# Optimization experiments

Measured on AMD Instinct MI355X. Metric: run time of the kernel, lower is better.

The kernel has to match this reference:

```python
import jax, jax.numpy as jnp
import numpy as np
from jax import lax

WIN = 11
SIGMA = 1.5
C1 = 0.01 ** 2
C2 = 0.03 ** 2


def _gauss_window(c):
    x = np.arange(WIN) - WIN // 2
    g = np.exp(-(x ** 2) / (2.0 * SIGMA ** 2))
    g = g / g.sum()
    w2d = np.outer(g, g).astype(np.float32)  # [11,11]
    return jnp.asarray(np.broadcast_to(w2d, (c, 1, WIN, WIN)).copy())


def _dwconv(x, kernel, groups):
    # x: [B,C,H,W], kernel: [C,1,kh,kw] depthwise, stride 1, SAME padding
    return lax.conv_general_dilated(
        x, kernel, window_strides=(1, 1), padding='SAME',
        dimension_numbers=('NCHW', 'OIHW', 'NCHW'),
        feature_group_count=groups)


_SOBEL_X = jnp.asarray(np.array([[-1, 0, 1], [-2, 0, 2], [-1, 0, 1]], np.float32))
_SOBEL_Y = jnp.asarray(np.array([[1, 2, 1], [0, 0, 0], [-1, -2, -1]], np.float32))


def _sobel_xy(x):
    # x: [B,3,H,W] -> depthwise 3x3 sobel on each channel (same as per-channel conv2d)
    c = x.shape[1]
    kx = jnp.broadcast_to(_SOBEL_X, (c, 1, 3, 3))
    ky = jnp.broadcast_to(_SOBEL_Y, (c, 1, 3, 3))
    return _dwconv(x, kx, c), _dwconv(x, ky, c)


def _rgb2ycrcb(im):
    R, G, B = im[:, 0:1], im[:, 1:2], im[:, 2:3]
    Y = 0.299 * R + 0.587 * G + 0.114 * B
    Cr = (R - Y) * 0.713 + 0.5
    Cb = (B - Y) * 0.564 + 0.5
    return Y, Cr, Cb


def _ssim(img1, img2, channel):
    w = _gauss_window(channel)
    mu1 = _dwconv(img1, w, channel)
    mu2 = _dwconv(img2, w, channel)
    mu1_sq = mu1 * mu1
    mu2_sq = mu2 * mu2
    mu12 = mu1 * mu2
    s1 = _dwconv(img1 * img1, w, channel) - mu1_sq
    s2 = _dwconv(img2 * img2, w, channel) - mu2_sq
    s12 = _dwconv(img1 * img2, w, channel) - mu12
    ssim_map = ((2 * mu12 + C1) * (2 * s12 + C2)) / ((mu1_sq + mu2_sq + C1) * (s1 + s2 + C2))
    return ssim_map.mean()


def _l1(a, b):
    return jnp.mean(jnp.abs(a - b))


def setup_inputs() -> dict:
    key = jax.random.key(0)
    k1, k2, k3 = jax.random.split(key, 3)
    shp = (16, 3, 512, 512)
    return {
        'input_vis': jax.random.uniform(k1, shp, jnp.float32),
        'input_ir': jax.random.uniform(k2, shp, jnp.float32),
        'fuse': jax.random.uniform(k3, shp, jnp.float32),
    }


def reference(input_vis, input_ir, fuse):
    # color components
    _, Cr_F, Cb_F = _rgb2ycrcb(fuse)
    _, Cr_V, Cb_V = _rgb2ycrcb(input_vis)
    Y_ir = input_ir[:, 0:1]

    # sobel gradients (depthwise over 3 channels == per-channel conv + cat)
    Fgx, Fgy = _sobel_xy(fuse)
    Vgx, Vgy = _sobel_xy(input_vis)
    Igx, Igy = _sobel_xy(input_ir)
    joint_gx = jnp.maximum(Vgx, Igx)
    joint_gy = jnp.maximum(Vgy, Igy)
    joint_int = jnp.maximum(input_vis, input_ir)

    con_loss = _l1(fuse, joint_int)
    gradient_loss = 0.5 * _l1(Fgx, joint_gx) + 0.5 * _l1(Fgy, joint_gy)
    color_loss = _l1(Cb_F, Cb_V) + _l1(Cr_F, Cr_V)

    # SSIM: rgb-vs-fused (3ch) and ir-Y vs gray(fused) (1ch)
    ssim_rgb = _ssim(input_vis, fuse, 3)
    gray_fused = (0.2989 * fuse[:, 0:1] + 0.587 * fuse[:, 1:2] + 0.114 * fuse[:, 2:3])
    ssim_ir = _ssim(Y_ir, gray_fused, 1)
    ssim_loss = 1.0 - (ssim_rgb + ssim_ir) / 2.0

    return 0.5 * con_loss + 0.2 * gradient_loss + 1.0 * color_loss + 0.1 * ssim_loss
```

## Files before the change

### kernel.cpp

```cpp
#include <hip/hip_runtime.h>

#define IMG_H 512
#define IMG_W 512
#define CH_STRIDE (IMG_H*IMG_W)
#define IMG_STRIDE (3*CH_STRIDE)

using f4 = __attribute__((ext_vector_type(4))) float;
using h4 = __attribute__((ext_vector_type(4))) _Float16;

#define NSLOT 64
#define SLOT_F 32

__global__ __launch_bounds__(256) void k_zero(float* __restrict__ acc) {
  int i = threadIdx.x;
  *(f4*)&acc[i*8]     = f4{0,0,0,0};
  *(f4*)&acc[i*8 + 4] = f4{0,0,0,0};
}

__device__ __forceinline__ float block_sum(float v, float* red) {
  #pragma unroll
  for (int o = 32; o > 0; o >>= 1) v += __shfl_down(v, o, 64);
  __syncthreads();
  if ((threadIdx.x & 63) == 0) red[threadIdx.x >> 6] = v;
  __syncthreads();
  return red[0] + red[1] + red[2] + red[3];
}

#define R1W 68
#define R1N (18*R1W)

#define SXW 80
#define SXH 42
#define HBW 68
#define HBN (SXH*HBW)

#define SMEM_BYTES 36288

__global__ __launch_bounds__(256, 4) void k_main(
    const float* __restrict__ vis, const float* __restrict__ ir,
    const float* __restrict__ fuse, float* __restrict__ acc)
{
  __shared__ __align__(16) char smem[SMEM_BYTES];
  __shared__ float red[4];
  const int tid = threadIdx.x;
  const int bid = blockIdx.x;
  float* aslot = acc + (bid & (NSLOT-1))*SLOT_F;

  if (bid < 8192) {
    const int z = bid >> 7;
    const int n = z >> 2, pair = z & 3;
    const int x0 = (bid & 7)*64;
    const int y0 = ((bid >> 3) & 15)*32;
    _Float16* sx = (_Float16*)smem;
    _Float16* sy = (_Float16*)(smem + 6720);
    _Float16* hA = (_Float16*)(smem + 13440);
    _Float16* hB = (_Float16*)(smem + 19152);
    _Float16* hP = (_Float16*)(smem + 24864);
    _Float16* hQ = (_Float16*)(smem + 30576);

    float g[11];
    {
      const float gu[6] = {0.00386592014f, 0.02856550078f, 0.13533528324f,
                           0.41111229050f, 0.80073740292f, 1.0f};
      float gs = 0.f;
      #pragma unroll
      for (int i = 0; i < 11; ++i) { g[i] = gu[i < 6 ? i : 10 - i]; gs += g[i]; }
      #pragma unroll
      for (int i = 0; i < 11; ++i) g[i] /= gs;
    }

    if (pair < 3) {
      const float* xb = vis  + (n*3 + pair)*CH_STRIDE;
      const float* yb = fuse + (n*3 + pair)*CH_STRIDE;
      for (int i = tid; i < SXH*20; i += 256) {
        int row = i / 20, k = i - row*20;
        int gy = y0 - 5 + row, gx = x0 - 8 + 4*k;
        f4 xv = {0,0,0,0}, yv = {0,0,0,0};
        if ((unsigned)gx < IMG_W && (unsigned)gy < IMG_H) {
          int off = gy*IMG_W + gx;
          xv = *(const f4*)&xb[off];
          yv = *(const f4*)&yb[off];
        }
        int ib = row*SXW + 4*k;
        *(h4*)&sx[ib] = h4{(_Float16)xv.x,(_Float16)xv.y,(_Float16)xv.z,(_Float16)xv.w};
        *(h4*)&sy[ib] = h4{(_Float16)yv.x,(_Float16)yv.y,(_Float16)yv.z,(_Float16)yv.w};
      }
    } else {
      const float* xb = ir   + n*IMG_STRIDE;
      const float* fb = fuse + n*IMG_STRIDE;
      for (int i = tid; i < SXH*20; i += 256) {
        int row = i / 20, k = i - row*20;
        int gy = y0 - 5 + row, gx = x0 - 8 + 4*k;
        f4 xv = {0,0,0,0}, yv = {0,0,0,0};
        if ((unsigned)gx < IMG_W && (unsigned)gy < IMG_H) {
          int off = gy*IMG_W + gx;
          xv = *(const f4*)&xb[off];
          f4 rr = *(const f4*)&fb[off];
          f4 gg = *(const f4*)&fb[off + CH_STRIDE];
          f4 bb = *(const f4*)&fb[off + 2*CH_STRIDE];
          #pragma unroll
          for (int j = 0; j < 4; ++j)
            yv[j] = 0.2989f*rr[j] + 0.587f*gg[j] + 0.114f*bb[j];
        }
        int ib = row*SXW + 4*k;
        *(h4*)&sx[ib] = h4{(_Float16)xv.x,(_Float16)xv.y,(_Float16)xv.z,(_Float16)xv.w};
        *(h4*)&sy[ib] = h4{(_Float16)yv.x,(_Float16)yv.y,(_Float16)yv.z,(_Float16)yv.w};
      }
    }
    __syncthreads();

    for (int gi = tid; gi < SXH*16; gi += 256) {
      int row = gi >> 4, gox = (gi & 15)*4;
      int base = row*SXW + gox;
      float wa[20], wb[20];
      #pragma unroll
      for (int u = 0; u < 5; ++u) {
        h4 av = *(const h4*)&sx[base + 4*u];
        h4 bv = *(const h4*)&sy[base + 4*u];
        #pragma unroll
        for (int j = 0; j < 4; ++j) { wa[4*u+j] = (float)av[j]; wb[4*u+j] = (float)bv[j]; }
      }
      float wp[14], wq[14];
      #pragma unroll
      for (int u = 0; u < 14; ++u) {
        float a = wa[u+3], b = wb[u+3];
        wp[u] = fmaf(a, a, b*b);
        wq[u] = a*b;
      }
      float hA4[4]={0,0,0,0}, hB4[4]={0,0,0,0}, hP4[4]={0,0,0,0}, hQ4[4]={0,0,0,0};
      #pragma unroll
      for (int k = 0; k < 11; ++k) {
        float gk = g[k];
        #pragma unroll
        for (int j = 0; j < 4; ++j) {
          hA4[j] = fmaf(gk, wa[k+j+3], hA4[j]);
          hB4[j] = fmaf(gk, wb[k+j+3], hB4[j]);
          hP4[j] = fmaf(gk, wp[k+j], hP4[j]);
          hQ4[j] = fmaf(gk, wq[k+j], hQ4[j]);
        }
      }
      int ob = row*HBW + gox;
      *(h4*)&hA[ob] = h4{(_Float16)hA4[0],(_Float16)hA4[1],(_Float16)hA4[2],(_Float16)hA4[3]};
      *(h4*)&hB[ob] = h4{(_Float16)hB4[0],(_Float16)hB4[1],(_Float16)hB4[2],(_Float16)hB4[3]};
      *(h4*)&hP[ob] = h4{(_Float16)hP4[0],(_Float16)hP4[1],(_Float16)hP4[2],(_Float16)hP4[3]};
      *(h4*)&hQ[ob] = h4{(_Float16)hQ4[0],(_Float16)hQ4[1],(_Float16)hQ4[2],(_Float16)hQ4[3]};
    }
    __syncthreads();

    const int vox = (tid & 15)*4;
    const int yb2 = (tid >> 4)*2;
    float aA0[4]={0,0,0,0}, aA1[4]={0,0,0,0};
    float aB0[4]={0,0,0,0}, aB1[4]={0,0,0,0};
    float aP0[4]={0,0,0,0}, aP1[4]={0,0,0,0};
    float aQ0[4]={0,0,0,0}, aQ1[4]={0,0,0,0};
    #pragma unroll
    for (int r = 0; r < 12; ++r) {
      int rb = (yb2 + r)*HBW + vox;
      h4 fA = *(const h4*)&hA[rb];
      h4 fB = *(const h4*)&hB[rb];
      h4 fP = *(const h4*)&hP[rb];
      h4 fQ = *(const h4*)&hQ[rb];
      if (r < 11) {
        float gk = g[r];
        #pragma unroll
        for (int j = 0; j < 4; ++j) {
          aA0[j] = fmaf(gk, (float)fA[j], aA0[j]);
          aB0[j] = fmaf(gk, (float)fB[j], aB0[j]);
          aP0[j] = fmaf(gk, (float)fP[j], aP0[j]);
          aQ0[j] = fmaf(gk, (float)fQ[j], aQ0[j]);
        }
      }
      if (r >= 1) {
        float gk = g[r-1];
        #pragma unroll
        for (int j = 0; j < 4; ++j) {
          aA1[j] = fmaf(gk, (float)fA[j], aA1[j]);
          aB1[j] = fmaf(gk, (float)fB[j], aB1[j]);
          aP1[j] = fmaf(gk, (float)fP[j], aP1[j]);
          aQ1[j] = fmaf(gk, (float)fQ[j], aQ1[j]);
        }
      }
    }

    float ss = 0.f;
    #pragma unroll
    for (int j = 0; j < 4; ++j) {
      {
        float mu1 = aA0[j], mu2 = aB0[j];
        float mu12 = mu1*mu2, mss = mu1*mu1 + mu2*mu2;
        float s12 = aQ0[j] - mu12, sps = aP0[j] - mss;
        ss += ((2.f*mu12 + 1e-4f)*(2.f*s12 + 9e-4f)) / ((mss + 1e-4f)*(sps + 9e-4f));
      }
      {
        float mu1 = aA1[j], mu2 = aB1[j];
        float mu12 = mu1*mu2, mss = mu1*mu1 + mu2*mu2;
        float s12 = aQ1[j] - mu12, sps = aP1[j] - mss;
        ss += ((2.f*mu12 + 1e-4f)*(2.f*s12 + 9e-4f)) / ((mss + 1e-4f)*(sps + 9e-4f));
      }
    }
    float tot = block_sum(ss, red);
    if (tid == 0) atomicAdd(&aslot[(pair == 3) ? 6 : 5], tot);

  } else {
    const int r = bid - 8192;
    const int x0 = (r & 7)*64;
    const int y0 = ((r >> 3) & 31)*16;
    const int n  = r >> 8;
    float* s = (float*)smem;
    const int ox = (tid & 15)*4;
    const int oy = tid >> 4;

    float con=0.f, gxs=0.f, gys=0.f, cbs=0.f, crs=0.f;
    float pv[3][4], pf[3][4];

    for (int c = 0; c < 3; ++c) {
      const float* pv0 = vis  + (n*3 + c)*CH_STRIDE;
      const float* pi0 = ir   + (n*3 + c)*CH_STRIDE;
      const float* pf0 = fuse + (n*3 + c)*CH_STRIDE;
      for (int i = tid; i < 864; i += 256) {
        int f = i / 288;
        int rr = i - f*288;
        int row = rr >> 4, k = rr & 15;
        int gy = y0 - 1 + row, gx = x0 + 4*k;
        f4 v = {0,0,0,0};
        const float* bp = (f == 0) ? pv0 : ((f == 1) ? pi0 : pf0);
        if ((unsigned)gy < IMG_H) v = *(const f4*)&bp[gy*IMG_W + gx];
        float* dst = s + f*R1N + row*R1W + 1 + 4*k;
        dst[0]=v.x; dst[1]=v.y; dst[2]=v.z; dst[3]=v.w;
      }
      if (tid < 108) {
        int f = tid / 36;
        int rr = tid - f*36;
        int row = rr >> 1, side = rr & 1;
        int gy = y0 - 1 + row;
        int gx = side ? (x0 + 64) : (x0 - 1);
        float v = 0.f;
        const float* bp = (f == 0) ? pv0 : ((f == 1) ? pi0 : pf0);
        if ((unsigned)gx < IMG_W && (unsigned)gy < IMG_H) v = bp[gy*IMG_W + gx];
        s[f*R1N + row*R1W + (side ? 65 : 0)] = v;
      }
      __syncthreads();

      float cen[3][4], gxv[3][4], gyv[3][4];
      #pragma unroll
      for (int t = 0; t < 3; ++t) {
        const float* sf = s + t*R1N;
        float r0[8], r1[8], r2[8];
        {
          f4 a = *(const f4*)&sf[(oy+0)*R1W + ox], b = *(const f4*)&sf[(oy+0)*R1W + ox + 4];
          r0[0]=a.x; r0[1]=a.y; r0[2]=a.z; r0[3]=a.w; r0[4]=b.x; r0[5]=b.y; r0[6]=b.z; r0[7]=b.w;
        }
        {
          f4 a = *(const f4*)&sf[(oy+1)*R1W + ox], b = *(const f4*)&sf[(oy+1)*R1W + ox + 4];
          r1[0]=a.x; r1[1]=a.y; r1[2]=a.z; r1[3]=a.w; r1[4]=b.x; r1[5]=b.y; r1[6]=b.z; r1[7]=b.w;
        }
        {
          f4 a = *(const f4*)&sf[(oy+2)*R1W + ox], b = *(const f4*)&sf[(oy+2)*R1W + ox + 4];
          r2[0]=a.x; r2[1]=a.y; r2[2]=a.z; r2[3]=a.w; r2[4]=b.x; r2[5]=b.y; r2[6]=b.z; r2[7]=b.w;
        }
        #pragma unroll
        for (int j = 0; j < 4; ++j) {
          gxv[t][j] = (r0[j+2]-r0[j]) + 2.f*(r1[j+2]-r1[j]) + (r2[j+2]-r2[j]);
          gyv[t][j] = (r0[j] + 2.f*r0[j+1] + r0[j+2]) - (r2[j] + 2.f*r2[j+1] + r2[j+2]);
          cen[t][j] = r1[j+1];
        }
      }
      #pragma unroll
      for (int j = 0; j < 4; ++j) {
        con += fabsf(cen[2][j] - fmaxf(cen[0][j], cen[1][j]));
        gxs += fabsf(gxv[2][j] - fmaxf(gxv[0][j], gxv[1][j]));
        gys += fabsf(gyv[2][j] - fmaxf(gyv[0][j], gyv[1][j]));
        pv[c][j] = cen[0][j];
        pf[c][j] = cen[2][j];
      }
      __syncthreads();
    }

    #pragma unroll
    for (int j = 0; j < 4; ++j) {
      float Yf = 0.299f*pf[0][j] + 0.587f*pf[1][j] + 0.114f*pf[2][j];
      float Yv = 0.299f*pv[0][j] + 0.587f*pv[1][j] + 0.114f*pv[2][j];
      crs += fabsf(0.713f*((pf[0][j]-Yf) - (pv[0][j]-Yv)));
      cbs += fabsf(0.564f*((pf[2][j]-Yf) - (pv[2][j]-Yv)));
    }

    float r0 = block_sum(con, red);
    float r1 = block_sum(gxs, red);
    float r2 = block_sum(gys, red);
    float r3 = block_sum(cbs, red);
    float r4 = block_sum(crs, red);
    if (tid == 0) {
      atomicAdd(&aslot[0], r0);
      atomicAdd(&aslot[1], r1);
      atomicAdd(&aslot[2], r2);
      atomicAdd(&aslot[3], r3);
      atomicAdd(&aslot[4], r4);
    }
  }
}

__global__ __launch_bounds__(64) void k_final(
    const float* __restrict__ acc, float* __restrict__ out)
{
  int lane = threadIdx.x;
  float s[7];
  #pragma unroll
  for (int c = 0; c < 7; ++c) {
    float x = acc[lane*SLOT_F + c];
    #pragma unroll
    for (int o = 32; o > 0; o >>= 1) x += __shfl_down(x, o, 64);
    s[c] = x;
  }
  if (lane == 0) {
    const float N3 = 16.f*3.f*512.f*512.f;
    const float N1 = 16.f*512.f*512.f;
    float con_loss  = s[0] / N3;
    float grad_loss = 0.5f*(s[1]/N3) + 0.5f*(s[2]/N3);
    float color_loss = s[3]/N1 + s[4]/N1;
    float ssim_loss = 1.f - (s[5]/N3 + s[6]/N1)*0.5f;
    out[0] = 0.5f*con_loss + 0.2f*grad_loss + color_loss + 0.1f*ssim_loss;
  }
}

extern "C" void kernel_launch(void* const* d_in, const int* in_sizes, int n_in,
                              void* d_out, int out_size, void* d_ws, size_t ws_size,
                              hipStream_t stream) {
  (void)in_sizes; (void)n_in; (void)out_size; (void)ws_size;
  const float* vis  = (const float*)d_in[0];
  const float* ir   = (const float*)d_in[1];
  const float* fuse = (const float*)d_in[2];
  float* out = (float*)d_out;
  float* acc = (float*)d_ws;

  k_zero<<<dim3(1,1,1), dim3(256,1,1), 0, stream>>>(acc);
  k_main<<<dim3(12288,1,1), dim3(256,1,1), 0, stream>>>(vis, ir, fuse, acc);
  k_final<<<dim3(1,1,1), dim3(64,1,1), 0, stream>>>(acc, out);
}
```

Measured before the change: 255.4 us.

## Compute separable SSIM Gaussian blur with MFMA banded-matrix multiplies

```diff
diff --git a/kernel.cpp b/kernel.cpp
--- a/kernel.cpp
+++ b/kernel.cpp
@@ -7,6 +7,7 @@
 
 using f4 = __attribute__((ext_vector_type(4))) float;
 using h4 = __attribute__((ext_vector_type(4))) _Float16;
+using h8 = __attribute__((ext_vector_type(8))) _Float16;
 
 #define NSLOT 64
 #define SLOT_F 32
@@ -29,12 +30,11 @@
 #define R1W 68
 #define R1N (18*R1W)
 
-#define SXW 80
-#define SXH 42
-#define HBW 68
-#define HBN (SXH*HBW)
-
-#define SMEM_BYTES 36288
+#define FST 104
+#define FSZ (48*FST*2)
+#define HTST 72
+#define HTSZ (64*HTST*2)
+#define SMEM_BYTES (2*FSZ + 2*HTSZ)
 
 __global__ __launch_bounds__(256, 4) void k_main(
     const float* __restrict__ vis, const float* __restrict__ ir,
@@ -42,6 +42,7 @@
 {
   __shared__ __align__(16) char smem[SMEM_BYTES];
   __shared__ float red[4];
+  __shared__ float gtab[96];
   const int tid = threadIdx.x;
   const int bid = blockIdx.x;
   float* aslot = acc + (bid & (NSLOT-1))*SLOT_F;
@@ -51,12 +52,10 @@
     const int n = z >> 2, pair = z & 3;
     const int x0 = (bid & 7)*64;
     const int y0 = ((bid >> 3) & 15)*32;
-    _Float16* sx = (_Float16*)smem;
-    _Float16* sy = (_Float16*)(smem + 6720);
-    _Float16* hA = (_Float16*)(smem + 13440);
-    _Float16* hB = (_Float16*)(smem + 19152);
-    _Float16* hP = (_Float16*)(smem + 24864);
-    _Float16* hQ = (_Float16*)(smem + 30576);
+    _Float16* FX  = (_Float16*)smem;
+    _Float16* FY  = (_Float16*)(smem + FSZ);
+    _Float16* HT0 = (_Float16*)(smem + 2*FSZ);
+    _Float16* HT1 = (_Float16*)(smem + 2*FSZ + HTSZ);
 
     float g[11];
     {
@@ -72,27 +71,27 @@
     if (pair < 3) {
       const float* xb = vis  + (n*3 + pair)*CH_STRIDE;
       const float* yb = fuse + (n*3 + pair)*CH_STRIDE;
-      for (int i = tid; i < SXH*20; i += 256) {
-        int row = i / 20, k = i - row*20;
+      for (int i = tid; i < 1152; i += 256) {
+        int row = i / 24, k = i - row*24;
         int gy = y0 - 5 + row, gx = x0 - 8 + 4*k;
         f4 xv = {0,0,0,0}, yv = {0,0,0,0};
-        if ((unsigned)gx < IMG_W && (unsigned)gy < IMG_H) {
+        if ((unsigned)gy < IMG_H && (unsigned)gx < IMG_W) {
           int off = gy*IMG_W + gx;
           xv = *(const f4*)&xb[off];
           yv = *(const f4*)&yb[off];
         }
-        int ib = row*SXW + 4*k;
-        *(h4*)&sx[ib] = h4{(_Float16)xv.x,(_Float16)xv.y,(_Float16)xv.z,(_Float16)xv.w};
-        *(h4*)&sy[ib] = h4{(_Float16)yv.x,(_Float16)yv.y,(_Float16)yv.z,(_Float16)yv.w};
+        int ib = row*FST + 4*k;
+        *(h4*)&FX[ib] = h4{(_Float16)xv.x,(_Float16)xv.y,(_Float16)xv.z,(_Float16)xv.w};
+        *(h4*)&FY[ib] = h4{(_Float16)yv.x,(_Float16)yv.y,(_Float16)yv.z,(_Float16)yv.w};
       }
     } else {
       const float* xb = ir   + n*IMG_STRIDE;
       const float* fb = fuse + n*IMG_STRIDE;
-      for (int i = tid; i < SXH*20; i += 256) {
-        int row = i / 20, k = i - row*20;
+      for (int i = tid; i < 1152; i += 256) {
+        int row = i / 24, k = i - row*24;
         int gy = y0 - 5 + row, gx = x0 - 8 + 4*k;
         f4 xv = {0,0,0,0}, yv = {0,0,0,0};
-        if ((unsigned)gx < IMG_W && (unsigned)gy < IMG_H) {
+        if ((unsigned)gy < IMG_H && (unsigned)gx < IMG_W) {
           int off = gy*IMG_W + gx;
           xv = *(const f4*)&xb[off];
           f4 rr = *(const f4*)&fb[off];
@@ -102,100 +101,109 @@
           for (int j = 0; j < 4; ++j)
             yv[j] = 0.2989f*rr[j] + 0.587f*gg[j] + 0.114f*bb[j];
         }
-        int ib = row*SXW + 4*k;
-        *(h4*)&sx[ib] = h4{(_Float16)xv.x,(_Float16)xv.y,(_Float16)xv.z,(_Float16)xv.w};
-        *(h4*)&sy[ib] = h4{(_Float16)yv.x,(_Float16)yv.y,(_Float16)yv.z,(_Float16)yv.w};
-      }
+        int ib = row*FST + 4*k;
+        *(h4*)&FX[ib] = h4{(_Float16)xv.x,(_Float16)xv.y,(_Float16)xv.z,(_Float16)xv.w};
+        *(h4*)&FY[ib] = h4{(_Float16)yv.x,(_Float16)yv.y,(_Float16)yv.z,(_Float16)yv.w};
+      }
+    }
+    if (tid < 96) gtab[tid] = 0.f;
+    #pragma unroll
+    for (int k = 0; k < 11; ++k) if (tid == 40 + k) gtab[40 + k] = g[k];
+    for (int i = tid; i < 512; i += 256) {
+      _Float16* HT = (i < 256) ? HT0 : HT1;
+      int r2 = i & 255;
+      int c = r2 >> 2, rseg = 48 + (r2 & 3)*4;
+      *(h4*)&HT[c*HTST + rseg] = h4{(_Float16)0.f,(_Float16)0.f,(_Float16)0.f,(_Float16)0.f};
     }
     __syncthreads();
 
-    for (int gi = tid; gi < SXH*16; gi += 256) {
-      int row = gi >> 4, gox = (gi & 15)*4;
-      int base = row*SXW + gox;
-      float wa[20], wb[20];
-      #pragma unroll
-      for (int u = 0; u < 5; ++u) {
-        h4 av = *(const h4*)&sx[base + 4*u];
-        h4 bv = *(const h4*)&sy[base + 4*u];
+    const int w  = tid >> 6;
+    const int l  = tid & 63;
+    const int q  = l >> 4;
+    const int li = l & 15;
+
+    const int Kbase = w >> 1;
+    const int nK = 1 + (w & 1);
+    h8 gxf[2];
+    #pragma unroll
+    for (int kk = 0; kk < 2; ++kk) {
+      h8 t = {0,0,0,0,0,0,0,0};
+      if (kk < nK) {
+        int idx0 = 40 + (Kbase + kk)*32 + q*8 - w*16 - li - 3;
         #pragma unroll
-        for (int j = 0; j < 4; ++j) { wa[4*u+j] = (float)av[j]; wb[4*u+j] = (float)bv[j]; }
-      }
-      float wp[14], wq[14];
-      #pragma unroll
-      for (int u = 0; u < 14; ++u) {
-        float a = wa[u+3], b = wb[u+3];
-        wp[u] = fmaf(a, a, b*b);
-        wq[u] = a*b;
-      }
-      float hA4[4]={0,0,0,0}, hB4[4]={0,0,0,0}, hP4[4]={0,0,0,0}, hQ4[4]={0,0,0,0};
-      #pragma unroll
-      for (int k = 0; k < 11; ++k) {
-        float gk = g[k];
+        for (int j = 0; j < 8; ++j) t[j] = (_Float16)gtab[idx0 + j];
+      }
+      gxf[kk] = t;
+    }
+    h8 gyA[3];
+    {
+      const int MK[3][2] = {{0,0},{1,0},{1,1}};
+      #pragma unroll
+      for (int p = 0; p < 3; ++p) {
+        int idx0 = 40 + MK[p][1]*32 + q*8 - MK[p][0]*16 - li;
+        h8 t;
         #pragma unroll
-        for (int j = 0; j < 4; ++j) {
-          hA4[j] = fmaf(gk, wa[k+j+3], hA4[j]);
-          hB4[j] = fmaf(gk, wb[k+j+3], hB4[j]);
-          hP4[j] = fmaf(gk, wp[k+j], hP4[j]);
-          hQ4[j] = fmaf(gk, wq[k+j], hQ4[j]);
-        }
-      }
-      int ob = row*HBW + gox;
-      *(h4*)&hA[ob] = h4{(_Float16)hA4[0],(_Float16)hA4[1],(_Float16)hA4[2],(_Float16)hA4[3]};
-      *(h4*)&hB[ob] = h4{(_Float16)hB4[0],(_Float16)hB4[1],(_Float16)hB4[2],(_Float16)hB4[3]};
-      *(h4*)&hP[ob] = h4{(_Float16)hP4[0],(_Float16)hP4[1],(_Float16)hP4[2],(_Float16)hP4[3]};
-      *(h4*)&hQ[ob] = h4{(_Float16)hQ4[0],(_Float16)hQ4[1],(_Float16)hQ4[2],(_Float16)hQ4[3]};
-    }
-    __syncthreads();
-
-    const int vox = (tid & 15)*4;
-    const int yb2 = (tid >> 4)*2;
-    float aA0[4]={0,0,0,0}, aA1[4]={0,0,0,0};
-    float aB0[4]={0,0,0,0}, aB1[4]={0,0,0,0};
-    float aP0[4]={0,0,0,0}, aP1[4]={0,0,0,0};
-    float aQ0[4]={0,0,0,0}, aQ1[4]={0,0,0,0};
-    #pragma unroll
-    for (int r = 0; r < 12; ++r) {
-      int rb = (yb2 + r)*HBW + vox;
-      h4 fA = *(const h4*)&hA[rb];
-      h4 fB = *(const h4*)&hB[rb];
-      h4 fP = *(const h4*)&hP[rb];
-      h4 fQ = *(const h4*)&hQ[rb];
-      if (r < 11) {
-        float gk = g[r];
-        #pragma unroll
-        for (int j = 0; j < 4; ++j) {
-          aA0[j] = fmaf(gk, (float)fA[j], aA0[j]);
-          aB0[j] = fmaf(gk, (float)fB[j], aB0[j]);
-          aP0[j] = fmaf(gk, (float)fP[j], aP0[j]);
-          aQ0[j] = fmaf(gk, (float)fQ[j], aQ0[j]);
-        }
-      }
-      if (r >= 1) {
-        float gk = g[r-1];
-        #pragma unroll
-        for (int j = 0; j < 4; ++j) {
-          aA1[j] = fmaf(gk, (float)fA[j], aA1[j]);
-          aB1[j] = fmaf(gk, (float)fB[j], aB1[j]);
-          aP1[j] = fmaf(gk, (float)fP[j], aP1[j]);
-          aQ1[j] = fmaf(gk, (float)fQ[j], aQ1[j]);
-        }
+        for (int j = 0; j < 8; ++j) t[j] = (_Float16)gtab[idx0 + j];
+        gyA[p] = t;
+      }
+    }
+
+    f4 accF[4][2];
+    #pragma unroll
+    for (int f = 0; f < 4; ++f)
+      #pragma unroll
+      for (int m = 0; m < 2; ++m) accF[f][m] = f4{0,0,0,0};
+
+    const int cw = w*16 + li;
+
+    for (int grp = 0; grp < 2; ++grp) {
+      if (grp) __syncthreads();
+      #pragma unroll
+      for (int M = 0; M < 3; ++M) {
+        f4 c0 = {0,0,0,0}, c1 = {0,0,0,0};
+        for (int kk = 0; kk < nK; ++kk) {
+          int K = Kbase + kk;
+          int fo = (M*16 + li)*FST + K*32 + q*8;
+          h8 ax = *(const h8*)(FX + fo);
+          h8 ay = *(const h8*)(FY + fo);
+          if (grp == 0) {
+            c0 = __builtin_amdgcn_mfma_f32_16x16x32_f16(ax, gxf[kk], c0, 0, 0, 0);
+            c1 = __builtin_amdgcn_mfma_f32_16x16x32_f16(ay, gxf[kk], c1, 0, 0, 0);
+          } else {
+            h8 ap = ax*ax + ay*ay;
+            h8 aq = ax*ay;
+            c0 = __builtin_amdgcn_mfma_f32_16x16x32_f16(ap, gxf[kk], c0, 0, 0, 0);
+            c1 = __builtin_amdgcn_mfma_f32_16x16x32_f16(aq, gxf[kk], c1, 0, 0, 0);
+          }
+        }
+        int ho = cw*HTST + M*16 + q*4;
+        *(h4*)(HT0 + ho) = h4{(_Float16)c0.x,(_Float16)c0.y,(_Float16)c0.z,(_Float16)c0.w};
+        *(h4*)(HT1 + ho) = h4{(_Float16)c1.x,(_Float16)c1.y,(_Float16)c1.z,(_Float16)c1.w};
+      }
+      __syncthreads();
+      #pragma unroll
+      for (int f = 0; f < 2; ++f) {
+        const _Float16* HT = f ? HT1 : HT0;
+        int fi = grp*2 + f;
+        h8 b0 = *(const h8*)(HT + cw*HTST + q*8);
+        accF[fi][0] = __builtin_amdgcn_mfma_f32_16x16x32_f16(gyA[0], b0, accF[fi][0], 0, 0, 0);
+        accF[fi][1] = __builtin_amdgcn_mfma_f32_16x16x32_f16(gyA[1], b0, accF[fi][1], 0, 0, 0);
+        h8 b1 = *(const h8*)(HT + cw*HTST + 32 + q*8);
+        accF[fi][1] = __builtin_amdgcn_mfma_f32_16x16x32_f16(gyA[2], b1, accF[fi][1], 0, 0, 0);
       }
     }
 
     float ss = 0.f;
     #pragma unroll
-    for (int j = 0; j < 4; ++j) {
-      {
-        float mu1 = aA0[j], mu2 = aB0[j];
+    for (int M = 0; M < 2; ++M) {
+      #pragma unroll
+      for (int r = 0; r < 4; ++r) {
+        float mu1 = accF[0][M][r], mu2 = accF[1][M][r];
+        float sP  = accF[2][M][r], sQ  = accF[3][M][r];
         float mu12 = mu1*mu2, mss = mu1*mu1 + mu2*mu2;
-        float s12 = aQ0[j] - mu12, sps = aP0[j] - mss;
-        ss += ((2.f*mu12 + 1e-4f)*(2.f*s12 + 9e-4f)) / ((mss + 1e-4f)*(sps + 9e-4f));
-      }
-      {
-        float mu1 = aA1[j], mu2 = aB1[j];
-        float mu12 = mu1*mu2, mss = mu1*mu1 + mu2*mu2;
-        float s12 = aQ1[j] - mu12, sps = aP1[j] - mss;
-        ss += ((2.f*mu12 + 1e-4f)*(2.f*s12 + 9e-4f)) / ((mss + 1e-4f)*(sps + 9e-4f));
+        float s12 = sQ - mu12, sps = sP - mss;
+        ss += ((2.f*mu12 + 1e-4f)*(2.f*s12 + 9e-4f)) /
+              ((mss + 1e-4f)*(sps + 9e-4f));
       }
     }
     float tot = block_sum(ss, red);
```

New measurement: 432.6 us. +69.4%, slower.

## Interleave SSIM horizontal-blur outputs and run vertical blur in packed fp16

Applied to the files above, without the earlier changes.

```diff
diff --git a/kernel.cpp b/kernel.cpp
--- a/kernel.cpp
+++ b/kernel.cpp
@@ -7,6 +7,7 @@
 
 using f4 = __attribute__((ext_vector_type(4))) float;
 using h4 = __attribute__((ext_vector_type(4))) _Float16;
+using h8 = __attribute__((ext_vector_type(8))) _Float16;
 
 #define NSLOT 64
 #define SLOT_F 32
@@ -26,15 +27,17 @@
   return red[0] + red[1] + red[2] + red[3];
 }
 
+__device__ __forceinline__ h8 splat8(_Float16 v) { return h8{v,v,v,v,v,v,v,v}; }
+
 #define R1W 68
 #define R1N (18*R1W)
 
 #define SXW 80
 #define SXH 42
-#define HBW 68
-#define HBN (SXH*HBW)
-
-#define SMEM_BYTES 36288
+#define HB8 264
+#define SSIM_SX_B (SXH*SXW*2)
+#define SSIM_HB_B (SXH*HB8*2)
+#define SMEM_BYTES (2*SSIM_SX_B + SSIM_HB_B)
 
 __global__ __launch_bounds__(256, 4) void k_main(
     const float* __restrict__ vis, const float* __restrict__ ir,
@@ -52,13 +55,11 @@
     const int x0 = (bid & 7)*64;
     const int y0 = ((bid >> 3) & 15)*32;
     _Float16* sx = (_Float16*)smem;
-    _Float16* sy = (_Float16*)(smem + 6720);
-    _Float16* hA = (_Float16*)(smem + 13440);
-    _Float16* hB = (_Float16*)(smem + 19152);
-    _Float16* hP = (_Float16*)(smem + 24864);
-    _Float16* hQ = (_Float16*)(smem + 30576);
+    _Float16* sy = (_Float16*)(smem + SSIM_SX_B);
+    _Float16* hb = (_Float16*)(smem + 2*SSIM_SX_B);
 
     float g[11];
+    _Float16 gh[11];
     {
       const float gu[6] = {0.00386592014f, 0.02856550078f, 0.13533528324f,
                            0.41111229050f, 0.80073740292f, 1.0f};
@@ -66,7 +67,7 @@
       #pragma unroll
       for (int i = 0; i < 11; ++i) { g[i] = gu[i < 6 ? i : 10 - i]; gs += g[i]; }
       #pragma unroll
-      for (int i = 0; i < 11; ++i) g[i] /= gs;
+      for (int i = 0; i < 11; ++i) { g[i] /= gs; gh[i] = (_Float16)g[i]; }
     }
 
     if (pair < 3) {
@@ -76,7 +77,7 @@
         int row = i / 20, k = i - row*20;
         int gy = y0 - 5 + row, gx = x0 - 8 + 4*k;
         f4 xv = {0,0,0,0}, yv = {0,0,0,0};
-        if ((unsigned)gx < IMG_W && (unsigned)gy < IMG_H) {
+        if ((unsigned)gy < IMG_H && (unsigned)gx < IMG_W) {
           int off = gy*IMG_W + gx;
           xv = *(const f4*)&xb[off];
           yv = *(const f4*)&yb[off];
@@ -92,7 +93,7 @@
         int row = i / 20, k = i - row*20;
         int gy = y0 - 5 + row, gx = x0 - 8 + 4*k;
         f4 xv = {0,0,0,0}, yv = {0,0,0,0};
-        if ((unsigned)gx < IMG_W && (unsigned)gy < IMG_H) {
+        if ((unsigned)gy < IMG_H && (unsigned)gx < IMG_W) {
           int off = gy*IMG_W + gx;
           xv = *(const f4*)&xb[off];
           f4 rr = *(const f4*)&fb[off];
@@ -109,93 +110,109 @@
     }
     __syncthreads();
 
-    for (int gi = tid; gi < SXH*16; gi += 256) {
-      int row = gi >> 4, gox = (gi & 15)*4;
-      int base = row*SXW + gox;
-      float wa[20], wb[20];
-      #pragma unroll
-      for (int u = 0; u < 5; ++u) {
-        h4 av = *(const h4*)&sx[base + 4*u];
-        h4 bv = *(const h4*)&sy[base + 4*u];
-        #pragma unroll
-        for (int j = 0; j < 4; ++j) { wa[4*u+j] = (float)av[j]; wb[4*u+j] = (float)bv[j]; }
-      }
-      float wp[14], wq[14];
-      #pragma unroll
-      for (int u = 0; u < 14; ++u) {
-        float a = wa[u+3], b = wb[u+3];
-        wp[u] = fmaf(a, a, b*b);
-        wq[u] = a*b;
-      }
-      float hA4[4]={0,0,0,0}, hB4[4]={0,0,0,0}, hP4[4]={0,0,0,0}, hQ4[4]={0,0,0,0};
-      #pragma unroll
-      for (int k = 0; k < 11; ++k) {
-        float gk = g[k];
-        #pragma unroll
-        for (int j = 0; j < 4; ++j) {
-          hA4[j] = fmaf(gk, wa[k+j+3], hA4[j]);
-          hB4[j] = fmaf(gk, wb[k+j+3], hB4[j]);
-          hP4[j] = fmaf(gk, wp[k+j], hP4[j]);
-          hQ4[j] = fmaf(gk, wq[k+j], hQ4[j]);
-        }
-      }
-      int ob = row*HBW + gox;
-      *(h4*)&hA[ob] = h4{(_Float16)hA4[0],(_Float16)hA4[1],(_Float16)hA4[2],(_Float16)hA4[3]};
-      *(h4*)&hB[ob] = h4{(_Float16)hB4[0],(_Float16)hB4[1],(_Float16)hB4[2],(_Float16)hB4[3]};
-      *(h4*)&hP[ob] = h4{(_Float16)hP4[0],(_Float16)hP4[1],(_Float16)hP4[2],(_Float16)hP4[3]};
-      *(h4*)&hQ[ob] = h4{(_Float16)hQ4[0],(_Float16)hQ4[1],(_Float16)hQ4[2],(_Float16)hQ4[3]};
+    for (int t = tid; t < SXH*8; t += 256) {
+      int row = t >> 3, p0 = (t & 7)*4;
+      int base = row*SXW + p0*2;
+      h8 xa0 = *(const h8*)&sx[base];
+      h8 xa1 = *(const h8*)&sx[base+8];
+      h8 xa2 = *(const h8*)&sx[base+16];
+      h8 yb0 = *(const h8*)&sy[base];
+      h8 yb1 = *(const h8*)&sy[base+8];
+      h8 yb2 = *(const h8*)&sy[base+16];
+      float wa[21], wb[21];
+      #pragma unroll
+      for (int u = 0; u < 21; ++u) {
+        wa[u] = (float)(u < 8 ? xa0[u] : (u < 16 ? xa1[u-8] : xa2[u-16]));
+        wb[u] = (float)(u < 8 ? yb0[u] : (u < 16 ? yb1[u-8] : yb2[u-16]));
+      }
+      h8 hA, hB, hP, hQ;
+      {
+        float a8[8] = {0,0,0,0,0,0,0,0};
+        #pragma unroll
+        for (int k = 0; k < 11; ++k) {
+          float gk = g[k];
+          #pragma unroll
+          for (int j = 0; j < 8; ++j) a8[j] = fmaf(gk, wa[3+k+j], a8[j]);
+        }
+        #pragma unroll
+        for (int j = 0; j < 8; ++j) hA[j] = (_Float16)a8[j];
+      }
+      {
+        float b8[8] = {0,0,0,0,0,0,0,0};
+        #pragma unroll
+        for (int k = 0; k < 11; ++k) {
+          float gk = g[k];
+          #pragma unroll
+          for (int j = 0; j < 8; ++j) b8[j] = fmaf(gk, wb[3+k+j], b8[j]);
+        }
+        #pragma unroll
+        for (int j = 0; j < 8; ++j) hB[j] = (_Float16)b8[j];
+      }
+      {
+        float wp[21];
+        #pragma unroll
+        for (int u = 3; u < 21; ++u) wp[u] = fmaf(wa[u], wa[u], wb[u]*wb[u]);
+        float p8[8] = {0,0,0,0,0,0,0,0};
+        #pragma unroll
+        for (int k = 0; k < 11; ++k) {
+          float gk = g[k];
+          #pragma unroll
+          for (int j = 0; j < 8; ++j) p8[j] = fmaf(gk, wp[3+k+j], p8[j]);
+        }
+        #pragma unroll
+        for (int j = 0; j < 8; ++j) hP[j] = (_Float16)p8[j];
+      }
+      {
+        float wq[21];
+        #pragma unroll
+        for (int u = 3; u < 21; ++u) wq[u] = wa[u]*wb[u];
+        float q8[8] = {0,0,0,0,0,0,0,0};
+        #pragma unroll
+        for (int k = 0; k < 11; ++k) {
+          float gk = g[k];
+          #pragma unroll
+          for (int j = 0; j < 8; ++j) q8[j] = fmaf(gk, wq[3+k+j], q8[j]);
+        }
+        #pragma unroll
+        for (int j = 0; j < 8; ++j) hQ[j] = (_Float16)q8[j];
+      }
+      #pragma unroll
+      for (int p = 0; p < 4; ++p) {
+        h8 o = h8{hA[2*p], hB[2*p], hP[2*p], hQ[2*p],
+                  hA[2*p+1], hB[2*p+1], hP[2*p+1], hQ[2*p+1]};
+        *(h8*)&hb[row*HB8 + (p0 + p)*8] = o;
+      }
     }
     __syncthreads();
 
-    const int vox = (tid & 15)*4;
-    const int yb2 = (tid >> 4)*2;
-    float aA0[4]={0,0,0,0}, aA1[4]={0,0,0,0};
-    float aB0[4]={0,0,0,0}, aB1[4]={0,0,0,0};
-    float aP0[4]={0,0,0,0}, aP1[4]={0,0,0,0};
-    float aQ0[4]={0,0,0,0}, aQ1[4]={0,0,0,0};
-    #pragma unroll
-    for (int r = 0; r < 12; ++r) {
-      int rb = (yb2 + r)*HBW + vox;
-      h4 fA = *(const h4*)&hA[rb];
-      h4 fB = *(const h4*)&hB[rb];
-      h4 fP = *(const h4*)&hP[rb];
-      h4 fQ = *(const h4*)&hQ[rb];
-      if (r < 11) {
-        float gk = g[r];
-        #pragma unroll
-        for (int j = 0; j < 4; ++j) {
-          aA0[j] = fmaf(gk, (float)fA[j], aA0[j]);
-          aB0[j] = fmaf(gk, (float)fB[j], aB0[j]);
-          aP0[j] = fmaf(gk, (float)fP[j], aP0[j]);
-          aQ0[j] = fmaf(gk, (float)fQ[j], aQ0[j]);
-        }
-      }
-      if (r >= 1) {
-        float gk = g[r-1];
-        #pragma unroll
-        for (int j = 0; j < 4; ++j) {
-          aA1[j] = fmaf(gk, (float)fA[j], aA1[j]);
-          aB1[j] = fmaf(gk, (float)fB[j], aB1[j]);
-          aP1[j] = fmaf(gk, (float)fP[j], aP1[j]);
-          aQ1[j] = fmaf(gk, (float)fQ[j], aQ1[j]);
-        }
+    const int xp = tid & 31;
+    const int ybase = (tid >> 5)*4;
+    h8 vacc[4];
+    #pragma unroll
+    for (int m = 0; m < 4; ++m) vacc[m] = splat8((_Float16)0.f);
+    #pragma unroll
+    for (int r = 0; r < 14; ++r) {
+      h8 rv = *(const h8*)&hb[(ybase + r)*HB8 + xp*8];
+      #pragma unroll
+      for (int m = 0; m < 4; ++m) {
+        int k = r - m;
+        if (k >= 0 && k < 11) vacc[m] += splat8(gh[k]) * rv;
       }
     }
 
     float ss = 0.f;
     #pragma unroll
-    for (int j = 0; j < 4; ++j) {
-      {
-        float mu1 = aA0[j], mu2 = aB0[j];
+    for (int m = 0; m < 4; ++m) {
+      #pragma unroll
+      for (int px = 0; px < 2; ++px) {
+        float mu1 = (float)vacc[m][4*px + 0];
+        float mu2 = (float)vacc[m][4*px + 1];
+        float sP  = (float)vacc[m][4*px + 2];
+        float sQ  = (float)vacc[m][4*px + 3];
         float mu12 = mu1*mu2, mss = mu1*mu1 + mu2*mu2;
-        float s12 = aQ0[j] - mu12, sps = aP0[j] - mss;
-        ss += ((2.f*mu12 + 1e-4f)*(2.f*s12 + 9e-4f)) / ((mss + 1e-4f)*(sps + 9e-4f));
-      }
-      {
-        float mu1 = aA1[j], mu2 = aB1[j];
-        float mu12 = mu1*mu2, mss = mu1*mu1 + mu2*mu2;
-        float s12 = aQ1[j] - mu12, sps = aP1[j] - mss;
-        ss += ((2.f*mu12 + 1e-4f)*(2.f*s12 + 9e-4f)) / ((mss + 1e-4f)*(sps + 9e-4f));
+        float s12 = sQ - mu12, sps = sP - mss;
+        ss += ((2.f*mu12 + 1e-4f)*(2.f*s12 + 9e-4f)) /
+              ((mss + 1e-4f)*(sps + 9e-4f));
       }
     }
     float tot = block_sum(ss, red);
```

After: 245.5 us. 1.04x faster.
